# Kernel tuning notes

Measured on AMD Instinct MI355X. Metric: run time of the kernel, lower is better.

## Reference

```python
import jax, jax.numpy as jnp
import numpy as np
from jax import lax

SCORE_THRESHOLD = 0.02
IOU_THRESHOLD = 0.5
NUM_CLASSES = 80
MAX_DETECTIONS = 10  # tf.image.non_max_suppression max_output_size in the source
ANCHORS = np.array([[1.08, 1.19], [3.42, 4.41], [6.63, 11.38], [9.42, 5.11], [16.62, 10.52]], dtype=np.float32)


def setup_inputs() -> dict:
    key = jax.random.key(0)
    k1, _ = jax.random.split(key)
    B, H, W = 16, 76, 76
    A = ANCHORS.shape[0]
    feats = jax.random.normal(k1, (B, H, W, A * (5 + NUM_CLASSES)), dtype=jnp.float32)
    anchors = jnp.asarray(ANCHORS)
    return {"feats": feats, "anchors": anchors}


def yolo_head(feats, anchors, num_classes):
    """Standard YOLOv2 decode (interpret_prediction)."""
    B, H, W, _ = feats.shape
    A = anchors.shape[0]
    feats = feats.reshape(B, H, W, A, 5 + num_classes)
    gy, gx = jnp.meshgrid(jnp.arange(H), jnp.arange(W), indexing="ij")
    grid = jnp.stack([gx, gy], axis=-1).astype(feats.dtype)  # [H,W,2] in (x,y) order
    conv_dims = jnp.array([W, H], dtype=feats.dtype)
    box_xy = (jax.nn.sigmoid(feats[..., 0:2]) + grid[None, :, :, None, :]) / conv_dims
    box_wh = jnp.exp(feats[..., 2:4]) * anchors[None, None, None, :, :] / conv_dims
    box_confidence = jax.nn.sigmoid(feats[..., 4:5])
    box_class_probs = jax.nn.softmax(feats[..., 5:], axis=-1)
    return box_xy, box_wh, box_confidence, box_class_probs


def _postprocess(feats, anchors):
    box_xy, box_wh, box_confidence, box_class_probs = yolo_head(feats, anchors, NUM_CLASSES)
    box_mins = box_xy - box_wh / 2.0
    box_maxes = box_xy + box_wh / 2.0
    # [y_min, x_min, y_max, x_max] as in the source (indices 1 then 0)
    boxes = jnp.concatenate([box_mins[..., 1:2], box_mins[..., 0:1], box_maxes[..., 1:2], box_maxes[..., 0:1]], axis=-1)
    box_scores = box_confidence * box_class_probs           # [B,H,W,A,C]
    box_classes = jnp.argmax(box_scores, axis=-1)           # [B,H,W,A]
    box_class_scores = jnp.max(box_scores, axis=-1)         # [B,H,W,A]

    # tf.boolean_mask flattens across all dims; emulate with fixed shapes by
    # marking below-threshold candidates as invalid (score -1).
    flat_boxes = boxes.reshape(-1, 4)                       # [N,4]
    flat_scores = box_class_scores.reshape(-1)              # [N]
    flat_classes = box_classes.reshape(-1)                  # [N]
    scores_work = jnp.where(flat_scores >= SCORE_THRESHOLD, flat_scores, -1.0)

    N = flat_boxes.shape[0]
    areas = jnp.maximum(flat_boxes[:, 2] - flat_boxes[:, 0], 0.0) * jnp.maximum(flat_boxes[:, 3] - flat_boxes[:, 1], 0.0)
    idx_range = jnp.arange(N)

    def step(sw, _):
        idx = jnp.argmax(sw)
        s = sw[idx]
        valid = s >= SCORE_THRESHOLD
        box = flat_boxes[idx]                               # [4] = y1,x1,y2,x2
        iy1 = jnp.maximum(box[0], flat_boxes[:, 0])
        ix1 = jnp.maximum(box[1], flat_boxes[:, 1])
        iy2 = jnp.minimum(box[2], flat_boxes[:, 2])
        ix2 = jnp.minimum(box[3], flat_boxes[:, 3])
        inter = jnp.maximum(iy2 - iy1, 0.0) * jnp.maximum(ix2 - ix1, 0.0)
        box_area = jnp.maximum(box[2] - box[0], 0.0) * jnp.maximum(box[3] - box[1], 0.0)
        iou = inter / (box_area + areas - inter + 1e-9)
        suppress = (iou > IOU_THRESHOLD) | (idx_range == idx)
        sw_new = jnp.where(valid & suppress, -1.0, sw)
        row = jnp.concatenate([box, s[None], flat_classes[idx].astype(jnp.float32)[None]])  # [6]
        row = jnp.where(valid, row, jnp.zeros_like(row))
        return sw_new, row

    _, rows = lax.scan(step, scores_work, None, length=MAX_DETECTIONS)
    return rows  # [MAX_DETECTIONS, 6] = [y1,x1,y2,x2,score,class]; zero rows are padding


def reference(feats, anchors):
    return _postprocess(feats, anchors)
```

## Files before the change

kernel.cpp:

```cpp
#include <hip/hip_runtime.h>
#include <stdint.h>

#define N_CAND 462080
#define NBINS  2048
#define HIST_BLOCKS 32
#define COMPACT_BLOCKS 64
#define TARGET 256u
#define SMAX   1024
#define SCORE_THR 0.02f
#define NB 7220
#define C_CNT 0
#define C_BIN 16
#define C_HD  32
#define C_CD  48


typedef const __attribute__((address_space(1))) uint32_t* gas1_u32;
typedef __attribute__((address_space(3))) uint32_t*       las3_u32;
#define GLOAD_LDS16(g, l) __builtin_amdgcn_global_load_lds( \
    (gas1_u32)(const void*)(g), (las3_u32)(void*)(l), 16, 0, 0)

__global__ __launch_bounds__(64) void decode_kernel(
    const float* __restrict__ feats,
    float* __restrict__ scores, unsigned char* __restrict__ cls,
    unsigned int* __restrict__ ctrl)
{
    __shared__ __align__(16) float lds[64 * 85];
    const int t = threadIdx.x;
    const int c = t & 31;
    const int h = t >> 5;

    if (blockIdx.x == 0 && t == 0) { ctrl[C_HD] = 0u; ctrl[C_CD] = 0u; }

    {
        const float4* __restrict__ src = (const float4*)(feats + (size_t)blockIdx.x * 5440);
        float4* dst = (float4*)lds;
#pragma unroll
        for (int i = 0; i < 10; ++i)
            GLOAD_LDS16(src + i * 64 + t, dst + i * 64 + t);
        if (t < 40) GLOAD_LDS16(src + 640 + t, dst + 640 + t);
#pragma unroll
        for (int i = 0; i < 10; ++i)
            GLOAD_LDS16(src + 680 + i * 64 + t, dst + 680 + i * 64 + t);
        if (t < 40) GLOAD_LDS16(src + 1320 + t, dst + 1320 + t);
    }

#pragma unroll
    for (int half = 0; half < 2; ++half) {
        if (half == 0)
            asm volatile("s_waitcnt vmcnt(11)" ::: "memory");
        else
            asm volatile("s_waitcnt vmcnt(0)" ::: "memory");
        __builtin_amdgcn_sched_barrier(0);

        const int cand = half * 32 + c;
        const float* f = lds + cand * 85;
        const int kb = 5 + h * 40;

        float m = f[kb];
        int cb = h * 40;
#pragma unroll
        for (int k = 1; k < 40; ++k) {
            float v = f[kb + k];
            if (v > m) { m = v; cb = h * 40 + k; }
        }
        float mo = __shfl_xor(m, 32);
        int   cbo = __shfl_xor(cb, 32);
        float m0 = (h == 0) ? m : mo,  m1 = (h == 0) ? mo : m;
        int   c0 = (h == 0) ? cb : cbo, c1 = (h == 0) ? cbo : cb;
        float mall = fmaxf(m0, m1);
        int   cls_abs = (m0 >= m1) ? c0 : c1;

        float s0 = 0.f, s1 = 0.f, s2 = 0.f, s3 = 0.f;
#pragma unroll
        for (int k = 0; k < 40; k += 4) {
            s0 += __expf(f[kb + k + 0] - mall);
            s1 += __expf(f[kb + k + 1] - mall);
            s2 += __expf(f[kb + k + 2] - mall);
            s3 += __expf(f[kb + k + 3] - mall);
        }
        float sl = (s0 + s1) + (s2 + s3);
        float sall = sl + __shfl_xor(sl, 32);

        if (h == 0) {
            const int ci = blockIdx.x * 64 + cand;
            float conf = 1.0f / (1.0f + __expf(-f[4]));
            float score = conf / sall;
            scores[ci] = (score >= SCORE_THR) ? score : -1.0f;
            cls[ci] = (unsigned char)cls_abs;
        }
    }
}

__global__ __launch_bounds__(1024) void hist_cutoff_kernel(
    const float* __restrict__ scores, unsigned short* __restrict__ hist_part,
    unsigned int* __restrict__ ctrl)
{
    __shared__ unsigned int lh[NBINS];
    __shared__ unsigned int pa[1024], pb[1024];
    __shared__ int lastf;
    const int t = threadIdx.x;

    lh[2 * t] = 0u; lh[2 * t + 1] = 0u;
    __syncthreads();

    for (int i = blockIdx.x * 1024 + t; i < N_CAND; i += HIST_BLOCKS * 1024) {
        float s = scores[i];
        if (s >= SCORE_THR) {
            int bin = (int)(s * (float)NBINS);
            bin = bin > (NBINS - 1) ? (NBINS - 1) : bin;
            atomicAdd(&lh[bin], 1u);
        }
    }
    __syncthreads();
    unsigned int* outp = (unsigned int*)(hist_part + (size_t)blockIdx.x * NBINS);
    outp[t] = (lh[2 * t] & 0xFFFFu) | (lh[2 * t + 1] << 16);
    __syncthreads();

    if (t == 0) {
        __threadfence();
        unsigned old = atomicAdd(&ctrl[C_HD], 1u);
        lastf = (old == HIST_BLOCKS - 1) ? 1 : 0;
    }
    __syncthreads();
    if (!lastf) return;
    if (t == 0) __threadfence();
    __syncthreads();

    const unsigned int* hp32 = (const unsigned int*)hist_part;
    unsigned b0 = 0u, b1 = 0u;
#pragma unroll 4
    for (int p = 0; p < HIST_BLOCKS; ++p) {
        unsigned v = hp32[p * 1024 + t];
        b0 += v & 0xFFFFu;
        b1 += v >> 16;
    }
    lh[2 * t] = b0; lh[2 * t + 1] = b1;
    pa[t] = b0 + b1;
    __syncthreads();

    unsigned int* srcb = pa; unsigned int* dstb = pb;
    for (int off = 1; off < 1024; off <<= 1) {
        unsigned v = srcb[t] + ((t + off < 1024) ? srcb[t + off] : 0u);
        dstb[t] = v;
        __syncthreads();
        unsigned int* tmp = srcb; srcb = dstb; dstb = tmp;
    }
    unsigned St = srcb[t];
    unsigned Sn = (t < 1023) ? srcb[t + 1] : 0u;

    if (t == 0) {
        ctrl[C_CNT] = 0u;
        if (St < TARGET) ctrl[C_BIN] = 0u;
    }
    if (St >= TARGET && Sn < TARGET) {
        unsigned run = Sn + lh[2 * t + 1];
        ctrl[C_BIN] = (run >= TARGET) ? (unsigned)(2 * t + 1) : (unsigned)(2 * t);
    }
}

__device__ inline float4 decode_box(const float* __restrict__ feats,
                                    const float* __restrict__ anchors, int ci)
{
    int a = ci % 5;
    int cell = ci / 5;
    int gx = cell % 76;
    int gy = (cell / 76) % 76;
    const float* f = feats + (long long)ci * 85;
    float bx = (1.0f / (1.0f + __expf(-f[0])) + (float)gx) / 76.0f;
    float by = (1.0f / (1.0f + __expf(-f[1])) + (float)gy) / 76.0f;
    float bw = __expf(f[2]) * anchors[2 * a]     / 76.0f;
    float bh = __expf(f[3]) * anchors[2 * a + 1] / 76.0f;
    return make_float4(by - bh * 0.5f, bx - bw * 0.5f,
                       by + bh * 0.5f, bx + bw * 0.5f);
}

__global__ __launch_bounds__(1024) void compact_nms_kernel(
    const float* __restrict__ scores, unsigned int* __restrict__ ctrl,
    float* __restrict__ lscore, int* __restrict__ lidx,
    const float* __restrict__ feats, const float* __restrict__ anchors,
    const unsigned char* __restrict__ cls, float* __restrict__ out)
{
    __shared__ unsigned long long wkey[16];
    __shared__ unsigned long long bkey;
    __shared__ float4 bbox;
    __shared__ int lastf;
    const int t = threadIdx.x;

    const int cut = (int)ctrl[C_BIN];
    for (int i = blockIdx.x * 1024 + t; i < N_CAND; i += COMPACT_BLOCKS * 1024) {
        float sw = scores[i];
        if (sw >= SCORE_THR) {
            int bin = (int)(sw * (float)NBINS);
            bin = bin > (NBINS - 1) ? (NBINS - 1) : bin;
            if (bin >= cut) {
                unsigned pos = atomicAdd(&ctrl[C_CNT], 1u);
                if (pos < SMAX) { lscore[pos] = sw; lidx[pos] = i; }
            }
        }
    }
    __syncthreads();
    if (t == 0) {
        __threadfence();
        unsigned old = atomicAdd(&ctrl[C_CD], 1u);
        lastf = (old == COMPACT_BLOCKS - 1) ? 1 : 0;
    }
    __syncthreads();
    if (!lastf) return;
    if (t == 0) __threadfence();
    __syncthreads();

    unsigned cnt = ctrl[C_CNT];
    int n = (cnt < (unsigned)SMAX) ? (int)cnt : SMAX;

    unsigned long long key = 0ull;
    float4 mb = make_float4(0.f, 0.f, 0.f, 0.f);
    float  msc = 0.f, mcls = 0.f;
    unsigned midx = 0xFFFFFFFFu;
    bool aliveb = false;
    if (t < n) {
        msc  = lscore[t];
        midx = (unsigned)lidx[t];
        key  = ((unsigned long long)__float_as_uint(msc) << 32)
             | (unsigned long long)(0xFFFFFFFFu - midx);
        mb   = decode_box(feats, anchors, (int)midx);
        mcls = (float)cls[midx];
        aliveb = true;
    }

    for (int r = 0; r < 10; ++r) {
        unsigned long long k0 = aliveb ? key : 0ull;
#pragma unroll
        for (int msk = 32; msk > 0; msk >>= 1) {
            unsigned long long o = __shfl_xor(k0, msk);
            k0 = (o > k0) ? o : k0;
        }
        if ((t & 63) == 0) wkey[t >> 6] = k0;
        __syncthreads();
        if (t < 16) {
            unsigned long long v = wkey[t];
#pragma unroll
            for (int msk = 8; msk > 0; msk >>= 1) {
                unsigned long long o = __shfl_xor(v, msk);
                v = (o > v) ? o : v;
            }
            if (t == 0) bkey = v;
        }
        __syncthreads();

        unsigned long long wk = bkey;
        bool have = (wk != 0ull);
        unsigned widx = have ? (0xFFFFFFFFu - (unsigned)(wk & 0xFFFFFFFFull)) : 0xFFFFFFFFu;

        if (have && aliveb && midx == widx) {
            bbox = mb;
            out[r * 6 + 0] = mb.x;
            out[r * 6 + 1] = mb.y;
            out[r * 6 + 2] = mb.z;
            out[r * 6 + 3] = mb.w;
            out[r * 6 + 4] = msc;
            out[r * 6 + 5] = mcls;
            aliveb = false;
        }
        if (!have && t == 0) {
#pragma unroll
            for (int q = 0; q < 6; ++q) out[r * 6 + q] = 0.f;
        }
        __syncthreads();

        if (have && aliveb) {
            float4 ab = bbox;
            float aarea = fmaxf(ab.z - ab.x, 0.f) * fmaxf(ab.w - ab.y, 0.f);
            float iy1 = fmaxf(ab.x, mb.x);
            float ix1 = fmaxf(ab.y, mb.y);
            float iy2 = fminf(ab.z, mb.z);
            float ix2 = fminf(ab.w, mb.w);
            float inter = fmaxf(iy2 - iy1, 0.f) * fmaxf(ix2 - ix1, 0.f);
            float carea = fmaxf(mb.z - mb.x, 0.f) * fmaxf(mb.w - mb.y, 0.f);
            float iou = inter / (aarea + carea - inter + 1e-9f);
            if (iou > 0.5f) aliveb = false;
        }
    }
}

extern "C" void kernel_launch(void* const* d_in, const int* in_sizes, int n_in,
                              void* d_out, int out_size, void* d_ws, size_t ws_size,
                              hipStream_t stream) {
    const float* feats   = (const float*)d_in[0];
    const float* anchors = (const float*)d_in[1];
    char* ws = (char*)d_ws;

    unsigned int*   ctrl      = (unsigned int*)(ws + 0);
    unsigned short* hist_part = (unsigned short*)(ws + 256);
    float*          lscore    = (float*)(ws + 131328);
    int*            lidx      = (int*)(ws + 135424);
    float*          scores    = (float*)(ws + 139520);
    unsigned char*  cls       = (unsigned char*)(ws + 1987840);
    float*          out       = (float*)d_out;

    decode_kernel      <<<NB, 64, 0, stream>>>(feats, scores, cls, ctrl);
    hist_cutoff_kernel <<<HIST_BLOCKS, 1024, 0, stream>>>(scores, hist_part, ctrl);
    compact_nms_kernel <<<COMPACT_BLOCKS, 1024, 0, stream>>>(scores, ctrl, lscore, lidx,
                                                             feats, anchors, cls, out);
}
```

Measured before the change: 59.76 us.

## Halve decode tiles and stage feats through registers instead of direct LDS loads

The decode kernel now handles 32 candidates per block instead of 64, launching twice as many blocks with half the LDS footprint. The global_load_lds direct-to-LDS path and its split-wait pipelining are replaced by ordinary float4 loads into registers followed by LDS stores. This aims to raise occupancy and spread the memory-bound decode over more blocks. In exchange it adds a register round-trip, more block launches, and drops the overlap between the two halves.

```diff
diff --git a/kernel.cpp b/kernel.cpp
--- a/kernel.cpp
+++ b/kernel.cpp
@@ -8,24 +8,20 @@
 #define TARGET 256u
 #define SMAX   1024
 #define SCORE_THR 0.02f
-#define NB 7220
+#define NT 14440
+#define TILEF 2720
 #define C_CNT 0
 #define C_BIN 16
 #define C_HD  32
 #define C_CD  48
 
 
-typedef const __attribute__((address_space(1))) uint32_t* gas1_u32;
-typedef __attribute__((address_space(3))) uint32_t*       las3_u32;
-#define GLOAD_LDS16(g, l) __builtin_amdgcn_global_load_lds( \
-    (gas1_u32)(const void*)(g), (las3_u32)(void*)(l), 16, 0, 0)
-
 __global__ __launch_bounds__(64) void decode_kernel(
     const float* __restrict__ feats,
     float* __restrict__ scores, unsigned char* __restrict__ cls,
     unsigned int* __restrict__ ctrl)
 {
-    __shared__ __align__(16) float lds[64 * 85];
+    __shared__ __align__(16) float lds[TILEF];
     const int t = threadIdx.x;
     const int c = t & 31;
     const int h = t >> 5;
@@ -33,62 +29,54 @@
     if (blockIdx.x == 0 && t == 0) { ctrl[C_HD] = 0u; ctrl[C_CD] = 0u; }
 
     {
-        const float4* __restrict__ src = (const float4*)(feats + (size_t)blockIdx.x * 5440);
+        const float4* __restrict__ src = (const float4*)(feats + (size_t)blockIdx.x * TILEF);
         float4* dst = (float4*)lds;
-#pragma unroll
-        for (int i = 0; i < 10; ++i)
-            GLOAD_LDS16(src + i * 64 + t, dst + i * 64 + t);
-        if (t < 40) GLOAD_LDS16(src + 640 + t, dst + 640 + t);
-#pragma unroll
-        for (int i = 0; i < 10; ++i)
-            GLOAD_LDS16(src + 680 + i * 64 + t, dst + 680 + i * 64 + t);
-        if (t < 40) GLOAD_LDS16(src + 1320 + t, dst + 1320 + t);
-    }
-
-#pragma unroll
-    for (int half = 0; half < 2; ++half) {
-        if (half == 0)
-            asm volatile("s_waitcnt vmcnt(11)" ::: "memory");
-        else
-            asm volatile("s_waitcnt vmcnt(0)" ::: "memory");
-        __builtin_amdgcn_sched_barrier(0);
-
-        const int cand = half * 32 + c;
-        const float* f = lds + cand * 85;
-        const int kb = 5 + h * 40;
-
-        float m = f[kb];
-        int cb = h * 40;
-#pragma unroll
-        for (int k = 1; k < 40; ++k) {
-            float v = f[kb + k];
-            if (v > m) { m = v; cb = h * 40 + k; }
-        }
-        float mo = __shfl_xor(m, 32);
-        int   cbo = __shfl_xor(cb, 32);
-        float m0 = (h == 0) ? m : mo,  m1 = (h == 0) ? mo : m;
-        int   c0 = (h == 0) ? cb : cbo, c1 = (h == 0) ? cbo : cb;
-        float mall = fmaxf(m0, m1);
-        int   cls_abs = (m0 >= m1) ? c0 : c1;
-
-        float s0 = 0.f, s1 = 0.f, s2 = 0.f, s3 = 0.f;
-#pragma unroll
-        for (int k = 0; k < 40; k += 4) {
-            s0 += __expf(f[kb + k + 0] - mall);
-            s1 += __expf(f[kb + k + 1] - mall);
-            s2 += __expf(f[kb + k + 2] - mall);
-            s3 += __expf(f[kb + k + 3] - mall);
-        }
-        float sl = (s0 + s1) + (s2 + s3);
-        float sall = sl + __shfl_xor(sl, 32);
-
-        if (h == 0) {
-            const int ci = blockIdx.x * 64 + cand;
-            float conf = 1.0f / (1.0f + __expf(-f[4]));
-            float score = conf / sall;
-            scores[ci] = (score >= SCORE_THR) ? score : -1.0f;
-            cls[ci] = (unsigned char)cls_abs;
-        }
+        float4 v[10];
+#pragma unroll
+        for (int i = 0; i < 10; ++i) v[i] = src[i * 64 + t];
+        float4 vt;
+        if (t < 40) vt = src[640 + t];
+#pragma unroll
+        for (int i = 0; i < 10; ++i) dst[i * 64 + t] = v[i];
+        if (t < 40) dst[640 + t] = vt;
+    }
+    asm volatile("s_waitcnt lgkmcnt(0)" ::: "memory");
+    __builtin_amdgcn_sched_barrier(0);
+
+    const float* f = lds + c * 85;
+    const int kb = 5 + h * 40;
+
+    float m = f[kb];
+    int cb = h * 40;
+#pragma unroll
+    for (int k = 1; k < 40; ++k) {
+        float v = f[kb + k];
+        if (v > m) { m = v; cb = h * 40 + k; }
+    }
+    float mo = __shfl_xor(m, 32);
+    int   cbo = __shfl_xor(cb, 32);
+    float m0 = (h == 0) ? m : mo,  m1 = (h == 0) ? mo : m;
+    int   c0 = (h == 0) ? cb : cbo, c1 = (h == 0) ? cbo : cb;
+    float mall = fmaxf(m0, m1);
+    int   cls_abs = (m0 >= m1) ? c0 : c1;
+
+    float s0 = 0.f, s1 = 0.f, s2 = 0.f, s3 = 0.f;
+#pragma unroll
+    for (int k = 0; k < 40; k += 4) {
+        s0 += __expf(f[kb + k + 0] - mall);
+        s1 += __expf(f[kb + k + 1] - mall);
+        s2 += __expf(f[kb + k + 2] - mall);
+        s3 += __expf(f[kb + k + 3] - mall);
+    }
+    float sl = (s0 + s1) + (s2 + s3);
+    float sall = sl + __shfl_xor(sl, 32);
+
+    if (h == 0) {
+        const int ci = blockIdx.x * 32 + c;
+        float conf = 1.0f / (1.0f + __expf(-f[4]));
+        float score = conf / sall;
+        scores[ci] = (score >= SCORE_THR) ? score : -1.0f;
+        cls[ci] = (unsigned char)cls_abs;
     }
 }
 
@@ -298,7 +286,7 @@
     unsigned char*  cls       = (unsigned char*)(ws + 1987840);
     float*          out       = (float*)d_out;
 
-    decode_kernel      <<<NB, 64, 0, stream>>>(feats, scores, cls, ctrl);
+    decode_kernel      <<<NT, 64, 0, stream>>>(feats, scores, cls, ctrl);
     hist_cutoff_kernel <<<HIST_BLOCKS, 1024, 0, stream>>>(scores, hist_part, ctrl);
     compact_nms_kernel <<<COMPACT_BLOCKS, 1024, 0, stream>>>(scores, ctrl, lscore, lidx,
                                                              feats, anchors, cls, out);
```

After: 58.55 us. -2.0%, faster.
